# Optimization experiments

Measured on AMD Instinct MI355X. Metric: run time of the kernel, lower is better.

Reference implementation:

```python
import jax, jax.numpy as jnp
import numpy as np
from functools import partial

B = 131072          # training_size (batch)
D_IN = 100          # init_shape
H = 50              # neurons
T = 100             # dimTimes
DT = 0.01           # dt = 1/100
GAMMA = 0.05        # gamma = 1/20
I0 = 0.12


def setup_inputs() -> dict:
    key = jax.random.key(0)
    ks = jax.random.split(key, 7)
    s = lambda fan_in: 1.0 / np.sqrt(fan_in)
    return {
        "x": jax.random.normal(ks[0], (B, D_IN), dtype=jnp.float32),
        "W0": jax.random.uniform(ks[1], (H, D_IN), jnp.float32, -s(D_IN), s(D_IN)),
        "b0": jax.random.uniform(ks[2], (H,), jnp.float32, -s(D_IN), s(D_IN)),
        "W1": jax.random.uniform(ks[3], (H, H), jnp.float32, -s(H), s(H)),
        "b1": jax.random.uniform(ks[4], (H,), jnp.float32, -s(H), s(H)),
        "W2": jax.random.uniform(ks[5], (T - 1, H), jnp.float32, -s(H), s(H)),
        "b2": jax.random.uniform(ks[6], (T - 1,), jnp.float32, -s(H), s(H)),
    }


def reference(x, W0, b0, W1, b1, W2, b2):
    # 3-layer MLP: 100 -> 50 -> 50 -> 99
    h = jax.nn.relu(x @ W0.T + b0)
    h = jax.nn.relu(h @ W1.T + b1)
    out = h @ W2.T + b2                      # [B, T-1] growth rates per step

    # Euler recurrence: I[:,k] = I[:,k-1] + dt*(out[:,k-1]*I*(1-I) - gamma*I)
    i0 = jnp.full((x.shape[0],), I0, dtype=out.dtype)

    def step(I_prev, o_k):
        I_new = I_prev + DT * (o_k * I_prev * (1.0 - I_prev) - GAMMA * I_prev)
        return I_new, I_new

    _, I_rest = jax.lax.scan(step, i0, out.T)   # I_rest: [T-1, B]
    I = jnp.concatenate([i0[:, None], I_rest.T], axis=1)  # [B, T]
    return I
```

## Files before the change

kernel.cpp:

```cpp
#include <hip/hip_runtime.h>
#include <stdint.h>

#define BB      131072
#define TT      100
#define DT_C    0.01f
#define GAMMA_C 0.05f
#define I0_C    0.12f

typedef short bf16x8 __attribute__((ext_vector_type(8)));
typedef float f32x4  __attribute__((ext_vector_type(4)));

#define F0_U16  0
#define F1_U16  (16*512)
#define F2_U16  (24*512)
#define NFRAG_U16 (38*512)

__device__ __forceinline__ uint16_t f2bf(float x) {
    uint32_t u = __builtin_bit_cast(uint32_t, x);
    return (uint16_t)((u + 0x7fffu + ((u >> 16) & 1u)) >> 16);
}

__device__ __forceinline__ uint32_t pk2(float a, float b) {
    uint32_t r;
    asm("v_cvt_pk_bf16_f32 %0, %1, %2" : "=v"(r) : "v"(a), "v"(b));
    return r;
}

__global__ void pack_kernel(const float* __restrict__ W0, const float* __restrict__ b0,
                            const float* __restrict__ W1, const float* __restrict__ b1,
                            const float* __restrict__ W2, const float* __restrict__ b2,
                            uint16_t* __restrict__ wsu)
{
    const int gid = blockIdx.x * blockDim.x + threadIdx.x;
    const int gsz = gridDim.x * blockDim.x;
    for (int idx = gid; idx < NFRAG_U16; idx += gsz) {
        int f = idx >> 9;
        int r = idx & 511;
        int L = r >> 3, j = r & 7;
        int k8 = ((L >> 4) << 3) + j;
        int n16 = L & 15;
        float v = 0.0f;
        if (f < 16) {
            int kc = f >> 2, nt = f & 3;
            int kk = kc * 32 + k8, nn = nt * 16 + n16;
            if (nn < 50) {
                if (kk < 100) v = W0[nn * 100 + kk];
                else if (kk == 100) v = b0[nn];
            }
        } else if (f < 24) {
            int g = f - 16; int kc = g >> 2, nt = g & 3;
            int kk = kc * 32 + k8, nn = nt * 16 + n16;
            if (nn < 50) {
                if (kk < 50) v = W1[nn * 50 + kk];
                else if (kk == 50) v = b1[nn];
            }
        } else {
            int g = f - 24; int kc = g / 7, nt = g % 7;
            int kk = kc * 32 + k8, nn = nt * 16 + n16;
            if (nn < 99) {
                if (kk < 50) v = DT_C * W2[nn * 50 + kk];
                else if (kk == 50) v = DT_C * b2[nn];
            }
        }
        wsu[idx] = f2bf(v);
    }
}

#define SLAB_F 3200

__global__ __launch_bounds__(256, 3) void net_kernel(
    const float* __restrict__ x,
    const void*  __restrict__ wsv,
    float* __restrict__ out)
{
    __shared__ float lds[4 * SLAB_F];
    const int tid  = threadIdx.x;
    const int wave = tid >> 6, lane = tid & 63;
    const int quad = lane >> 4, l15 = lane & 15;
    float* slabF = lds + wave * SLAB_F;
    uint16_t* h0u = (uint16_t*)slabF;
    uint16_t* h1u = (uint16_t*)slabF + 32 * 88;
    const uint16_t* wsu = (const uint16_t*)wsv;

    const int row0 = (blockIdx.x * 4 + wave) * 32;

    bf16x8 a0[2][4];
    #pragma unroll
    for (int h = 0; h < 2; ++h) {
        const float* xrow = x + (size_t)(row0 + h * 16 + l15) * 100;
        #pragma unroll
        for (int kc = 0; kc < 3; ++kc) {
            f32x4 p = *(const f32x4*)(xrow + kc * 32 + quad * 8);
            f32x4 q = *(const f32x4*)(xrow + kc * 32 + quad * 8 + 4);
            union { bf16x8 v; uint32_t u[4]; } t;
            t.u[0] = pk2(p[0], p[1]); t.u[1] = pk2(p[2], p[3]);
            t.u[2] = pk2(q[0], q[1]); t.u[3] = pk2(q[2], q[3]);
            a0[h][kc] = t.v;
        }
        union { bf16x8 v; uint32_t u[4]; } t;
        t.u[0] = t.u[1] = t.u[2] = t.u[3] = 0u;
        if (quad == 0) {
            f32x4 p = *(const f32x4*)(xrow + 96);
            t.u[0] = pk2(p[0], p[1]); t.u[1] = pk2(p[2], p[3]);
            t.u[2] = 0x00003f80u;
        }
        a0[h][3] = t.v;
    }

    f32x4 acc0[2][4];
    #pragma unroll
    for (int h = 0; h < 2; ++h)
        #pragma unroll
        for (int nt = 0; nt < 4; ++nt) acc0[h][nt] = (f32x4){0.f, 0.f, 0.f, 0.f};
    #pragma unroll
    for (int kc = 0; kc < 4; ++kc) {
        #pragma unroll
        for (int nt = 0; nt < 4; ++nt) {
            bf16x8 b = ((const bf16x8*)(wsu + F0_U16 + (kc * 4 + nt) * 512))[lane];
            acc0[0][nt] = __builtin_amdgcn_mfma_f32_16x16x32_bf16(a0[0][kc], b, acc0[0][nt], 0, 0, 0);
            acc0[1][nt] = __builtin_amdgcn_mfma_f32_16x16x32_bf16(a0[1][kc], b, acc0[1][nt], 0, 0, 0);
        }
    }
    const bool is50 = (l15 == 2);
    #pragma unroll
    for (int h = 0; h < 2; ++h) {
        #pragma unroll
        for (int nt = 0; nt < 4; ++nt) {
            const int n = nt * 16 + l15;
            #pragma unroll
            for (int r2 = 0; r2 < 4; r2 += 2) {
                float v0 = fmaxf(acc0[h][nt][r2], 0.0f);
                float v1 = fmaxf(acc0[h][nt][r2 + 1], 0.0f);
                if (nt == 3 && is50) { v0 = 1.0f; v1 = 1.0f; }
                uint32_t p = pk2(v0, v1);
                const int m = h * 16 + quad * 4 + r2;
                h0u[m * 88 + n]       = (uint16_t)p;
                h0u[(m + 1) * 88 + n] = (uint16_t)(p >> 16);
            }
        }
    }

    bf16x8 a1[2][2];
    #pragma unroll
    for (int h = 0; h < 2; ++h)
        #pragma unroll
        for (int kc = 0; kc < 2; ++kc)
            a1[h][kc] = *(const bf16x8*)(h0u + (h * 16 + l15) * 88 + kc * 32 + quad * 8);

    f32x4 acc1[2][4];
    #pragma unroll
    for (int h = 0; h < 2; ++h)
        #pragma unroll
        for (int nt = 0; nt < 4; ++nt) acc1[h][nt] = (f32x4){0.f, 0.f, 0.f, 0.f};
    #pragma unroll
    for (int kc = 0; kc < 2; ++kc) {
        #pragma unroll
        for (int nt = 0; nt < 4; ++nt) {
            bf16x8 b = ((const bf16x8*)(wsu + F1_U16 + (kc * 4 + nt) * 512))[lane];
            acc1[0][nt] = __builtin_amdgcn_mfma_f32_16x16x32_bf16(a1[0][kc], b, acc1[0][nt], 0, 0, 0);
            acc1[1][nt] = __builtin_amdgcn_mfma_f32_16x16x32_bf16(a1[1][kc], b, acc1[1][nt], 0, 0, 0);
        }
    }
    #pragma unroll
    for (int h = 0; h < 2; ++h) {
        #pragma unroll
        for (int nt = 0; nt < 4; ++nt) {
            const int n = nt * 16 + l15;
            #pragma unroll
            for (int r2 = 0; r2 < 4; r2 += 2) {
                float v0 = fmaxf(acc1[h][nt][r2], 0.0f);
                float v1 = fmaxf(acc1[h][nt][r2 + 1], 0.0f);
                if (nt == 3 && is50) { v0 = 1.0f; v1 = 1.0f; }
                uint32_t p = pk2(v0, v1);
                const int m = h * 16 + quad * 4 + r2;
                h1u[m * 88 + n]       = (uint16_t)p;
                h1u[(m + 1) * 88 + n] = (uint16_t)(p >> 16);
            }
        }
    }

    bf16x8 a2[2][2];
    #pragma unroll
    for (int h = 0; h < 2; ++h)
        #pragma unroll
        for (int kc = 0; kc < 2; ++kc)
            a2[h][kc] = *(const bf16x8*)(h1u + (h * 16 + l15) * 88 + kc * 32 + quad * 8);

    f32x4 acc2[2][7];
    #pragma unroll
    for (int h = 0; h < 2; ++h)
        #pragma unroll
        for (int nt = 0; nt < 7; ++nt) acc2[h][nt] = (f32x4){0.f, 0.f, 0.f, 0.f};
    #pragma unroll
    for (int kc = 0; kc < 2; ++kc) {
        #pragma unroll
        for (int nt = 0; nt < 7; ++nt) {
            bf16x8 b = ((const bf16x8*)(wsu + F2_U16 + (kc * 7 + nt) * 512))[lane];
            acc2[0][nt] = __builtin_amdgcn_mfma_f32_16x16x32_bf16(a2[0][kc], b, acc2[0][nt], 0, 0, 0);
            acc2[1][nt] = __builtin_amdgcn_mfma_f32_16x16x32_bf16(a2[1][kc], b, acc2[1][nt], 0, 0, 0);
        }
    }
    #pragma unroll
    for (int h = 0; h < 2; ++h) {
        #pragma unroll
        for (int nt = 0; nt < 7; ++nt) {
            const int t = nt * 16 + l15;
            if (nt < 6 || l15 < 3) {
                #pragma unroll
                for (int r = 0; r < 4; ++r)
                    slabF[(h * 16 + quad * 4 + r) * 100 + t] = acc2[h][nt][r];
            }
        }
    }

    if (lane < 32) {
        float* orow = slabF + lane * 100;
        const float c = 1.0f - DT_C * GAMMA_C;
        float prev = I0_C;
        #pragma unroll
        for (int k = 1; k < TT; ++k) {
            const float op = orow[k - 1];
            const float s = c + op;
            orow[k - 1] = prev;
            prev = prev * fmaf(-op, prev, s);
        }
        orow[TT - 1] = prev;
    }

    float* gout = out + (size_t)row0 * 100;
    #pragma unroll
    for (int q = 0; q < 13; ++q) {
        const int i = q * 64 + lane;
        if (i < 800) {
            f32x4 v = *(const f32x4*)(slabF + 4 * i);
            __builtin_nontemporal_store(v, (f32x4*)(gout + 4 * i));
        }
    }
}

extern "C" void kernel_launch(void* const* d_in, const int* in_sizes, int n_in,
                              void* d_out, int out_size, void* d_ws, size_t ws_size,
                              hipStream_t stream) {
    const float* x  = (const float*)d_in[0];
    const float* W0 = (const float*)d_in[1];
    const float* b0 = (const float*)d_in[2];
    const float* W1 = (const float*)d_in[3];
    const float* b1 = (const float*)d_in[4];
    const float* W2 = (const float*)d_in[5];
    const float* b2 = (const float*)d_in[6];
    float* out = (float*)d_out;
    uint16_t* wsu = (uint16_t*)d_ws;

    pack_kernel<<<dim3(80), dim3(256), 0, stream>>>(W0, b0, W1, b1, W2, b2, wsu);
    net_kernel<<<dim3(BB / 128), dim3(256), 0, stream>>>(x, (const void*)wsu, out);
}
```

Measured before the change: 121.6 us.

## Halve per-wave LDS slab, process output halves sequentially, raise occupancy

The per-wave LDS slab is halved to 1600 floats by reusing one hidden-activation buffer for both layers. The final output is now handled in two 16-row halves: each half is written to LDS, runs the Euler recurrence on 16 lanes, and is stored to global memory. Launch bounds rise to 4 blocks per CU so more waves can hide latency. The recurrence now preloads its LDS reads in chunks of 25, and the x loads use nontemporal hints. In exchange, only 16 lanes run the serial recurrence at a time, done twice per wave, and register pressure may tighten under the higher occupancy target.

```diff
diff --git a/kernel.cpp b/kernel.cpp
--- a/kernel.cpp
+++ b/kernel.cpp
@@ -66,9 +66,9 @@
     }
 }
 
-#define SLAB_F 3200
-
-__global__ __launch_bounds__(256, 3) void net_kernel(
+#define SLAB_F 1600
+
+__global__ __launch_bounds__(256, 4) void net_kernel(
     const float* __restrict__ x,
     const void*  __restrict__ wsv,
     float* __restrict__ out)
@@ -78,8 +78,7 @@
     const int wave = tid >> 6, lane = tid & 63;
     const int quad = lane >> 4, l15 = lane & 15;
     float* slabF = lds + wave * SLAB_F;
-    uint16_t* h0u = (uint16_t*)slabF;
-    uint16_t* h1u = (uint16_t*)slabF + 32 * 88;
+    uint16_t* hu = (uint16_t*)slabF;
     const uint16_t* wsu = (const uint16_t*)wsv;
 
     const int row0 = (blockIdx.x * 4 + wave) * 32;
@@ -90,8 +89,8 @@
         const float* xrow = x + (size_t)(row0 + h * 16 + l15) * 100;
         #pragma unroll
         for (int kc = 0; kc < 3; ++kc) {
-            f32x4 p = *(const f32x4*)(xrow + kc * 32 + quad * 8);
-            f32x4 q = *(const f32x4*)(xrow + kc * 32 + quad * 8 + 4);
+            f32x4 p = __builtin_nontemporal_load((const f32x4*)(xrow + kc * 32 + quad * 8));
+            f32x4 q = __builtin_nontemporal_load((const f32x4*)(xrow + kc * 32 + quad * 8 + 4));
             union { bf16x8 v; uint32_t u[4]; } t;
             t.u[0] = pk2(p[0], p[1]); t.u[1] = pk2(p[2], p[3]);
             t.u[2] = pk2(q[0], q[1]); t.u[3] = pk2(q[2], q[3]);
@@ -100,7 +99,7 @@
         union { bf16x8 v; uint32_t u[4]; } t;
         t.u[0] = t.u[1] = t.u[2] = t.u[3] = 0u;
         if (quad == 0) {
-            f32x4 p = *(const f32x4*)(xrow + 96);
+            f32x4 p = __builtin_nontemporal_load((const f32x4*)(xrow + 96));
             t.u[0] = pk2(p[0], p[1]); t.u[1] = pk2(p[2], p[3]);
             t.u[2] = 0x00003f80u;
         }
@@ -134,8 +133,8 @@
                 if (nt == 3 && is50) { v0 = 1.0f; v1 = 1.0f; }
                 uint32_t p = pk2(v0, v1);
                 const int m = h * 16 + quad * 4 + r2;
-                h0u[m * 88 + n]       = (uint16_t)p;
-                h0u[(m + 1) * 88 + n] = (uint16_t)(p >> 16);
+                hu[m * 88 + n]       = (uint16_t)p;
+                hu[(m + 1) * 88 + n] = (uint16_t)(p >> 16);
             }
         }
     }
@@ -145,7 +144,7 @@
     for (int h = 0; h < 2; ++h)
         #pragma unroll
         for (int kc = 0; kc < 2; ++kc)
-            a1[h][kc] = *(const bf16x8*)(h0u + (h * 16 + l15) * 88 + kc * 32 + quad * 8);
+            a1[h][kc] = *(const bf16x8*)(hu + (h * 16 + l15) * 88 + kc * 32 + quad * 8);
 
     f32x4 acc1[2][4];
     #pragma unroll
@@ -173,8 +172,8 @@
                 if (nt == 3 && is50) { v0 = 1.0f; v1 = 1.0f; }
                 uint32_t p = pk2(v0, v1);
                 const int m = h * 16 + quad * 4 + r2;
-                h1u[m * 88 + n]       = (uint16_t)p;
-                h1u[(m + 1) * 88 + n] = (uint16_t)(p >> 16);
+                hu[m * 88 + n]       = (uint16_t)p;
+                hu[(m + 1) * 88 + n] = (uint16_t)(p >> 16);
             }
         }
     }
@@ -184,7 +183,7 @@
     for (int h = 0; h < 2; ++h)
         #pragma unroll
         for (int kc = 0; kc < 2; ++kc)
-            a2[h][kc] = *(const bf16x8*)(h1u + (h * 16 + l15) * 88 + kc * 32 + quad * 8);
+            a2[h][kc] = *(const bf16x8*)(hu + (h * 16 + l15) * 88 + kc * 32 + quad * 8);
 
     f32x4 acc2[2][7];
     #pragma unroll
@@ -200,6 +199,8 @@
             acc2[1][nt] = __builtin_amdgcn_mfma_f32_16x16x32_bf16(a2[1][kc], b, acc2[1][nt], 0, 0, 0);
         }
     }
+
+    const float cmul = 1.0f - DT_C * GAMMA_C;
     #pragma unroll
     for (int h = 0; h < 2; ++h) {
         #pragma unroll
@@ -208,32 +209,41 @@
             if (nt < 6 || l15 < 3) {
                 #pragma unroll
                 for (int r = 0; r < 4; ++r)
-                    slabF[(h * 16 + quad * 4 + r) * 100 + t] = acc2[h][nt][r];
-            }
-        }
-    }
-
-    if (lane < 32) {
-        float* orow = slabF + lane * 100;
-        const float c = 1.0f - DT_C * GAMMA_C;
-        float prev = I0_C;
-        #pragma unroll
-        for (int k = 1; k < TT; ++k) {
-            const float op = orow[k - 1];
-            const float s = c + op;
-            orow[k - 1] = prev;
-            prev = prev * fmaf(-op, prev, s);
-        }
-        orow[TT - 1] = prev;
-    }
-
-    float* gout = out + (size_t)row0 * 100;
-    #pragma unroll
-    for (int q = 0; q < 13; ++q) {
-        const int i = q * 64 + lane;
-        if (i < 800) {
-            f32x4 v = *(const f32x4*)(slabF + 4 * i);
-            __builtin_nontemporal_store(v, (f32x4*)(gout + 4 * i));
+                    slabF[(quad * 4 + r) * 100 + t] = acc2[h][nt][r];
+            }
+        }
+
+        if (lane < 16) {
+            float* orow = slabF + lane * 100;
+            float prev = I0_C;
+            #pragma unroll
+            for (int cch = 0; cch < 4; ++cch) {
+                const int n = (cch == 3) ? 24 : 25;
+                float buf[25];
+                #pragma unroll
+                for (int j = 0; j < 25; ++j)
+                    if (j < n) buf[j] = orow[cch * 25 + j];
+                #pragma unroll
+                for (int j = 0; j < 25; ++j) {
+                    if (j < n) {
+                        const float op = buf[j];
+                        const float s = cmul + op;
+                        orow[cch * 25 + j] = prev;
+                        prev = prev * fmaf(-op, prev, s);
+                    }
+                }
+            }
+            orow[TT - 1] = prev;
+        }
+
+        float* gout = out + (size_t)(row0 + h * 16) * 100;
+        #pragma unroll
+        for (int q = 0; q < 7; ++q) {
+            const int i = q * 64 + lane;
+            if (i < 400) {
+                f32x4 v = *(const f32x4*)(slabF + 4 * i);
+                __builtin_nontemporal_store(v, (f32x4*)(gout + 4 * i));
+            }
         }
     }
 }
```

New measurement: 128.7 us. 1.06x slower.
